# Optimization experiments

Measured on AMD Instinct MI355X. Metric: run time of the kernel, lower is better.

Reference implementation:

```python
import math
import jax, jax.numpy as jnp
import numpy as np

L, B, D = 2048, 8, 1024
Z, H, N = 128, 2048, 16


def setup_inputs() -> dict:
    key = jax.random.key(0)
    ks = jax.random.split(key, 16)
    s = 0.02
    inp = {
        "x": jax.random.normal(ks[0], (L, B, D), jnp.float32),
        "ln_w": jnp.ones((D,), jnp.float32),
        "ln_b": jnp.zeros((D,), jnp.float32),
        "v_w": jax.random.normal(ks[1], (H, D), jnp.float32) * s,
        "v_b": jnp.zeros((H,), jnp.float32),
        "mx_w": jax.random.normal(ks[2], (Z + H + 2 * D, D), jnp.float32) * s,
        "mx_b": jnp.zeros((Z + H + 2 * D,), jnp.float32),
        "h_w": jax.random.normal(ks[3], (D, H), jnp.float32) * s,
        "h_b": jnp.zeros((D,), jnp.float32),
        "qk_gamma": jnp.ones((2, Z), jnp.float32) + jax.random.normal(ks[4], (2, Z), jnp.float32) * s,
        "qk_beta": jax.random.normal(ks[5], (2, Z), jnp.float32) * s,
        "ema_delta": jax.random.normal(ks[6], (D, N, 1), jnp.float32),
        "ema_alpha": jax.random.normal(ks[7], (D, N, 1), jnp.float32),
        "ema_beta": jax.random.normal(ks[8], (D, N, 1), jnp.float32) * s,
        "ema_gamma": jax.random.normal(ks[9], (D, N), jnp.float32) * s,
        "ema_omega": jax.random.normal(ks[10], (D,), jnp.float32) * s,
        "rb_alpha": jax.random.normal(ks[11], (1, Z), jnp.float32) * s,
        "rb_beta": jax.random.normal(ks[12], (1, Z), jnp.float32) * s,
    }
    return inp


def _rotary_bias(rb_alpha, rb_beta, seq_len, z):
    # RotaryRelativePositionalBias.forward(seq_len) -> (L, L)
    half = z // 2
    freqs = jnp.exp(jnp.arange(half, dtype=jnp.float32) * (-math.log(10000.0) / half))
    pos = jnp.arange(seq_len, dtype=jnp.float32)[:, None] * freqs[None, :]  # (L, half)
    sin, cos = jnp.sin(pos), jnp.cos(pos)

    def rot(w):  # (1, Z) -> (L, Z)
        we = jnp.broadcast_to(w, (seq_len, z))
        w1, w2 = we[:, :half], we[:, half:]
        return jnp.concatenate([w1 * cos - w2 * sin, w2 * cos + w1 * sin], axis=1)

    return rot(rb_alpha) @ rot(rb_beta).T  # (L, L)


def _ema(xn, ema_delta, ema_alpha, ema_beta, ema_gamma, ema_omega):
    # xn: (L, B, D) -> damped multi-head EMA via FFT causal conv (MEGA MultiHeadEMA)
    seq_len = xn.shape[0]
    p = jax.nn.sigmoid(ema_delta)           # (D, N, 1)
    a = jax.nn.sigmoid(ema_alpha)           # (D, N, 1)
    q = 1.0 - p * a                         # (D, N, 1)
    t = jnp.arange(seq_len, dtype=jnp.float32)[None, None, :]
    kern = (p * ema_beta) * jnp.exp(t * jnp.log(q))          # (D, N, L)
    scale = math.sqrt(1.0 / kern.shape[1])
    k_dl = jnp.einsum("dnl,dn->dl", kern, ema_gamma * scale)  # (D, L)
    xt = jnp.transpose(xn, (1, 2, 0))        # (B, D, L)
    nfft = 2 * seq_len
    kf = jnp.fft.rfft(k_dl, n=nfft)          # (D, F)
    xf = jnp.fft.rfft(xt, n=nfft)            # (B, D, F)
    conv = jnp.fft.irfft(xf * kf, n=nfft)[..., :seq_len]      # (B, D, L)
    return jax.nn.silu(jnp.transpose(conv, (2, 0, 1)) + xn * ema_omega)  # (L, B, D)


def reference(x, ln_w, ln_b, v_w, v_b, mx_w, mx_b, h_w, h_b, qk_gamma, qk_beta,
              ema_delta, ema_alpha, ema_beta, ema_gamma, ema_omega, rb_alpha, rb_beta):
    seq_len, bsz, d = x.shape
    residual = x
    # prenorm LayerNorm
    mu = jnp.mean(x, axis=-1, keepdims=True)
    var = jnp.mean(jnp.square(x - mu), axis=-1, keepdims=True)
    xn = (x - mu) * jax.lax.rsqrt(var + 1e-5) * ln_w + ln_b

    v = jax.nn.silu(xn @ v_w.T + v_b)                          # (L, B, H)
    mx = _ema(xn, ema_delta, ema_alpha, ema_beta, ema_gamma, ema_omega)
    base = mx @ mx_w.T + mx_b                                  # (L, B, Z+H+2D)
    u = jax.nn.sigmoid(base[..., :d])                          # update gate
    zr = jax.nn.silu(base[..., d:d + Z + H])
    hx = base[..., d + Z + H:]
    z, r = zr[..., :Z], zr[..., Z:]                            # (L,B,Z), (L,B,H)
    z2 = z[:, :, None, :] * qk_gamma + qk_beta                 # (L, B, 2, Z)
    q = jnp.transpose(z2[:, :, 0], (1, 0, 2)) * (Z ** -0.5)    # (B, L, Z)
    k = jnp.transpose(z2[:, :, 1], (1, 0, 2))                  # (B, L, Z)
    vb = jnp.transpose(v, (1, 0, 2))                           # (B, L, H)

    bias = _rotary_bias(rb_alpha, rb_beta, seq_len, Z)         # (L, L)
    attn = jax.nn.softmax(jnp.einsum("blz,bmz->blm", q, k) + bias, axis=-1)
    h = jnp.transpose(jnp.einsum("blm,bmh->blh", attn, vb), (1, 0, 2))  # (L, B, H)
    h = jax.nn.silu(hx + (h * r) @ h_w.T + h_b)                # (L, B, D)
    return residual + u * (h - residual)
```

## Files before the change

### kernel.cpp

```cpp
#include <hip/hip_runtime.h>
#include <cstdint>
#include <cstddef>

typedef __bf16 bf16;
typedef __bf16 bf16x8 __attribute__((ext_vector_type(8)));
typedef float  f32x4  __attribute__((ext_vector_type(4)));

#define DEVI static __device__ __forceinline__

DEVI float fsigmoid(float x) { return 1.0f / (1.0f + __expf(-x)); }
DEVI float fsilu(float x)    { return x / (1.0f + __expf(-x)); }

DEVI unsigned short b16bits(float v) { bf16 h = (bf16)v; return __builtin_bit_cast(unsigned short, h); }
DEVI float lo16f(unsigned int w) { return __builtin_bit_cast(float, w << 16); }
DEVI float hi16f(unsigned int w) { return __builtin_bit_cast(float, w & 0xffff0000u); }

DEVI float waveRedSum(float v) {
#pragma unroll
  for (int o = 32; o > 0; o >>= 1) v += __shfl_xor(v, o, 64);
  return v;
}
DEVI float waveRedMax(float v) {
#pragma unroll
  for (int o = 32; o > 0; o >>= 1) v = fmaxf(v, __shfl_xor(v, o, 64));
  return v;
}

DEVI void xcd_swizzle(int& bx, int& by) {
  const int gx = gridDim.x, gy = gridDim.y;
  const int nwg = gx * gy;
  const int flat = blockIdx.y * gx + blockIdx.x;
  const int xcd = flat & 7;
  const int rem = nwg & 7;
  const int q = nwg >> 3;
  const int base = (xcd < rem) ? xcd * (q + 1) : rem * (q + 1) + (xcd - rem) * q;
  const int swz = base + (flat >> 3);
  bx = swz % gx;
  by = swz / gx;
}

struct alignas(8) B4 { bf16 x, y, z, w; };

__global__ __launch_bounds__(256) void k_copyout(const float* __restrict__ x, float* __restrict__ o)
{
  const long i = (long)blockIdx.x * 256 + threadIdx.x;
  ((float4*)o)[i] = ((const float4*)x)[i];
}

__global__ __launch_bounds__(256) void k_lnstats(const float* __restrict__ x, float* __restrict__ stats)
{
  const long t = blockIdx.x;
  const int tid = threadIdx.x;
  const float4 v = ((const float4*)(x + t * 1024))[tid];
  float s  = v.x + v.y + v.z + v.w;
  float s2 = v.x * v.x + v.y * v.y + v.z * v.z + v.w * v.w;
  __shared__ float red[2][4];
  s = waveRedSum(s);
  s2 = waveRedSum(s2);
  const int wv = tid >> 6, ln = tid & 63;
  if (ln == 0) { red[0][wv] = s; red[1][wv] = s2; }
  __syncthreads();
  if (tid == 0) {
    s  = red[0][0] + red[0][1] + red[0][2] + red[0][3];
    s2 = red[1][0] + red[1][1] + red[1][2] + red[1][3];
    const float mu  = s * (1.0f / 1024.0f);
    const float var = s2 * (1.0f / 1024.0f) - mu * mu;
    stats[2 * t]     = mu;
    stats[2 * t + 1] = rsqrtf(var + 1e-5f);
  }
}

__global__ __launch_bounds__(256) void k_cvt(const float* __restrict__ in, bf16* __restrict__ out, int n4)
{
  const int i = blockIdx.x * 256 + threadIdx.x;
  if (i >= n4) return;
  const float4 v = ((const float4*)in)[i];
  B4 h; h.x = (bf16)v.x; h.y = (bf16)v.y; h.z = (bf16)v.z; h.w = (bf16)v.w;
  ((B4*)out)[i] = h;
}

__global__ __launch_bounds__(256) void k_ema_coeff(
    const float* __restrict__ de, const float* __restrict__ al,
    const float* __restrict__ be, const float* __restrict__ ga,
    float* __restrict__ qv, float* __restrict__ cv)
{
  const int i = blockIdx.x * 256 + threadIdx.x;
  const int d = i >> 4, n = i & 15;
  const float p = 1.0f / (1.0f + expf(-de[i]));
  const float a = 1.0f / (1.0f + expf(-al[i]));
  qv[n * 1024 + d] = 1.0f - p * a;
  cv[n * 1024 + d] = p * be[i] * ga[i] * 0.25f;
}

__global__ __launch_bounds__(256) void k_ema_scan1(
    const float* __restrict__ x, const float* __restrict__ stats,
    const float* __restrict__ lnw, const float* __restrict__ lnb,
    const float* __restrict__ qv, float* __restrict__ scan)
{
  const int d = blockIdx.x * 256 + threadIdx.x;
  const int b = blockIdx.y, c = blockIdx.z;
  float q[16], s[16];
#pragma unroll
  for (int n = 0; n < 16; ++n) { q[n] = qv[n * 1024 + d]; s[n] = 0.0f; }
  const float wd = lnw[d], bd = lnb[d];
  const float* xp = x + (long)b * 1024 + d;
  const int l0 = c * 128;
  for (int j0 = 0; j0 < 128; j0 += 8) {
    float xr[8]; float2 st[8];
#pragma unroll
    for (int i = 0; i < 8; ++i) {
      const int l = l0 + j0 + i;
      xr[i] = xp[(long)l * 8192];
      st[i] = ((const float2*)stats)[(long)l * 8 + b];
    }
#pragma unroll
    for (int i = 0; i < 8; ++i) {
      const float xv = (xr[i] - st[i].x) * st[i].y * wd + bd;
#pragma unroll
      for (int n = 0; n < 16; ++n) s[n] = fmaf(q[n], s[n], xv);
    }
  }
  float* sp = scan + ((((long)c * 8 + b) * 1024) + d) * 16;
#pragma unroll
  for (int n = 0; n < 16; ++n) sp[n] = s[n];
}

__global__ __launch_bounds__(256) void k_ema_scan2(
    const float* __restrict__ qv, float* __restrict__ scan)
{
  const int i = blockIdx.x * 256 + threadIdx.x;
  const int n = i & 15, d = (i >> 4) & 1023, b = i >> 14;
  const float q = qv[n * 1024 + d];
  const float q2 = q * q, q4 = q2 * q2, q8 = q4 * q4;
  const float q16 = q8 * q8, q32 = q16 * q16, q64 = q32 * q32, q128 = q64 * q64;
  float carry = 0.0f;
#pragma unroll
  for (int c = 0; c < 16; ++c) {
    const long off = ((((long)c * 8 + b) * 1024) + d) * 16 + n;
    const float t = scan[off];
    scan[off] = carry;
    carry = fmaf(q128, carry, t);
  }
}

__global__ __launch_bounds__(256) void k_ema_apply(
    const float* __restrict__ x, const float* __restrict__ stats,
    const float* __restrict__ lnw, const float* __restrict__ lnb,
    const float* __restrict__ qv, const float* __restrict__ cv,
    const float* __restrict__ omega, const float* __restrict__ scan,
    bf16* __restrict__ mx)
{
  const int d = blockIdx.x * 256 + threadIdx.x;
  const int b = blockIdx.y, c = blockIdx.z;
  float q[16], cc[16], s[16];
  const float* sp = scan + ((((long)c * 8 + b) * 1024) + d) * 16;
#pragma unroll
  for (int n = 0; n < 16; ++n) {
    q[n] = qv[n * 1024 + d];
    cc[n] = cv[n * 1024 + d];
    s[n] = sp[n];
  }
  const float om = omega[d], wd = lnw[d], bd = lnb[d];
  const float* xp = x + (long)b * 1024 + d;
  bf16* mp = mx + (long)b * 1024 + d;
  const int l0 = c * 128;
  for (int j0 = 0; j0 < 128; j0 += 8) {
    float xr[8]; float2 st[8];
#pragma unroll
    for (int i = 0; i < 8; ++i) {
      const int l = l0 + j0 + i;
      xr[i] = xp[(long)l * 8192];
      st[i] = ((const float2*)stats)[(long)l * 8 + b];
    }
#pragma unroll
    for (int i = 0; i < 8; ++i) {
      const float xv = (xr[i] - st[i].x) * st[i].y * wd + bd;
      float p0 = 0.f, p1 = 0.f, p2 = 0.f, p3 = 0.f;
#pragma unroll
      for (int n = 0; n < 16; n += 4) {
        s[n]     = fmaf(q[n],     s[n],     xv);
        s[n + 1] = fmaf(q[n + 1], s[n + 1], xv);
        s[n + 2] = fmaf(q[n + 2], s[n + 2], xv);
        s[n + 3] = fmaf(q[n + 3], s[n + 3], xv);
        p0 = fmaf(cc[n],     s[n],     p0);
        p1 = fmaf(cc[n + 1], s[n + 1], p1);
        p2 = fmaf(cc[n + 2], s[n + 2], p2);
        p3 = fmaf(cc[n + 3], s[n + 3], p3);
      }
      const float pre = fmaf(xv, om, (p0 + p1) + (p2 + p3));
      mp[(long)(l0 + j0 + i) * 8192] = (bf16)fsilu(pre);
    }
  }
}

__global__ __launch_bounds__(64) void k_rotfill(
    const float* __restrict__ rba, const float* __restrict__ rbb,
    bf16* __restrict__ Qp, bf16* __restrict__ Kp)
{
  const int l = blockIdx.x, zi = threadIdx.x;
  const float fr = __expf(-0.14391156831212787f * (float)zi);
  const float pos = (float)l * fr;
  const float sn = sinf(pos), cs = cosf(pos);
  const float a1 = rba[zi], a2 = rba[64 + zi];
  const float b1 = rbb[zi], b2 = rbb[64 + zi];
  const bf16 qa = (bf16)(a1 * cs - a2 * sn);
  const bf16 qb = (bf16)(a2 * cs + a1 * sn);
  const bf16 ka = (bf16)(b1 * cs - b2 * sn);
  const bf16 kb = (bf16)(b2 * cs + b1 * sn);
#pragma unroll
  for (int b = 0; b < 8; ++b) {
    const long base = ((long)b * 2048 + l) * 256;
    Qp[base + 128 + zi] = qa;
    Qp[base + 192 + zi] = qb;
    Kp[base + 128 + zi] = ka;
    Kp[base + 192 + zi] = kb;
  }
}

__global__ __launch_bounds__(256) void k_softmax(float* __restrict__ S)
{
  const long row = blockIdx.x;
  float* sp = S + row * 2048;
  const int tid = threadIdx.x;
  float vals[8];
  float mx = -1e30f;
#pragma unroll
  for (int i = 0; i < 8; ++i) { vals[i] = sp[i * 256 + tid]; mx = fmaxf(mx, vals[i]); }
  __shared__ float red[4];
  mx = waveRedMax(mx);
  const int wv = tid >> 6, ln = tid & 63;
  if (ln == 0) red[wv] = mx;
  __syncthreads();
  mx = fmaxf(fmaxf(red[0], red[1]), fmaxf(red[2], red[3]));
  float sum = 0.f;
#pragma unroll
  for (int i = 0; i < 8; ++i) { vals[i] = __expf(vals[i] - mx); sum += vals[i]; }
  __syncthreads();
  sum = waveRedSum(sum);
  if (ln == 0) red[wv] = sum;
  __syncthreads();
  sum = red[0] + red[1] + red[2] + red[3];
  const float inv = 1.0f / sum;
  bf16* pp = (bf16*)sp;
#pragma unroll
  for (int i = 0; i < 8; ++i) pp[i * 256 + tid] = (bf16)(vals[i] * inv);
}

__global__ __launch_bounds__(1024) void k_vtrans8(
    const bf16* __restrict__ v, bf16* __restrict__ vt, const int loff)
{
  __shared__ bf16 tile[32][33];
  const int l0 = blockIdx.x * 32, h0 = blockIdx.y * 32, b = blockIdx.z;
  const int tx = threadIdx.x, ty = threadIdx.y;
  tile[ty][tx] = v[((long)(l0 + ty) * 8 + b) * 2048 + h0 + tx];
  __syncthreads();
  vt[((long)b * 2048 + h0 + ty) * 2048 + loff + l0 + tx] = tile[tx][ty];
}

DEVI void gload16(const void* g, void* l) {
  __builtin_amdgcn_global_load_lds(
      (__attribute__((address_space(1))) void*)(void*)g,
      (__attribute__((address_space(3))) void*)l, 16, 0, 0);
}

template<int EPI>
__global__ __launch_bounds__(256) void k_gemm_bt(
    const bf16* __restrict__ A, const bf16* __restrict__ Bm,
    const int K, const int lda, const int ldb, const int coladd,
    const float* __restrict__ bias,
    void* __restrict__ o0, void* __restrict__ o1, void* __restrict__ o2, void* __restrict__ o3,
    const void* __restrict__ e0, const void* __restrict__ e1, const void* __restrict__ e2)
{
  __shared__ alignas(16) bf16 As[128 * 64];
  __shared__ alignas(16) bf16 Bs[128 * 64];
  const int tid = threadIdx.x;
  const int wave = tid >> 6, lane = tid & 63;
  const int wm = wave >> 1, wn = wave & 1;
  int bx, by;
  xcd_swizzle(bx, by);
  const int tm = by * 128, tn = bx * 128;
  const int fr = lane & 15, kg = lane >> 4;

  f32x4 acc[4][4];
  const f32x4 z4 = {0.0f, 0.0f, 0.0f, 0.0f};
#pragma unroll
  for (int i = 0; i < 4; ++i)
#pragma unroll
    for (int j = 0; j < 4; ++j) acc[i][j] = z4;

  const int srow = wave * 8 + (lane >> 3);
  const int scol = ((lane & 7) ^ (lane >> 3)) * 8;
  const long arow = (long)(tm + srow);
  const long brow = (long)(tn + srow);
  const int swR = (fr & 7) << 3;

  for (int k0 = 0; k0 < K; k0 += 64) {
    __syncthreads();
#pragma unroll
    for (int cc = 0; cc < 4; ++cc) {
      gload16(A + (arow + cc * 32) * lda + k0 + scol, As + cc * 2048 + wave * 512);
      gload16(Bm + (brow + cc * 32) * ldb + k0 + scol, Bs + cc * 2048 + wave * 512);
    }
    __syncthreads();
    bf16x8 af[2][4], bfv[2][4];
#pragma unroll
    for (int ks = 0; ks < 2; ++ks)
#pragma unroll
      for (int i = 0; i < 4; ++i) {
        af[ks][i]  = *(const bf16x8*)&As[(wm * 64 + i * 16 + fr) * 64 + ((ks * 32 + kg * 8) ^ swR)];
        bfv[ks][i] = *(const bf16x8*)&Bs[(wn * 64 + i * 16 + fr) * 64 + ((ks * 32 + kg * 8) ^ swR)];
      }
#pragma unroll
    for (int ks = 0; ks < 2; ++ks)
#pragma unroll
      for (int i = 0; i < 4; ++i)
#pragma unroll
        for (int j = 0; j < 4; ++j)
          acc[i][j] = __builtin_amdgcn_mfma_f32_16x16x32_bf16(af[ks][i], bfv[ks][j], acc[i][j], 0, 0, 0);
  }

#pragma unroll
  for (int i = 0; i < 4; ++i) {
#pragma unroll
    for (int j = 0; j < 4; ++j) {
#pragma unroll
      for (int rr = 0; rr < 4; ++rr) {
        const int row = tm + wm * 64 + i * 16 + kg * 4 + rr;
        const int col = coladd + tn + wn * 64 + j * 16 + fr;
        const float a = acc[i][j][rr];
        if constexpr (EPI == 1) {
          const float tv = a + bias[col];
          if (col < 1024) {
            ((unsigned short*)o0)[((long)row * 1024 + col) * 2] = b16bits(fsigmoid(tv));
          } else if (col < 1152) {
            const int zi = col - 1024;
            const float zval = fsilu(tv);
            const float qq = (zval * ((const float*)e0)[zi] + ((const float*)e1)[zi]) * 0.08838834764831845f;
            const float kk =  zval * ((const float*)e0)[128 + zi] + ((const float*)e1)[128 + zi];
            const long base = ((long)(row & 7) * 2048 + (row >> 3)) * 256 + zi;
            ((bf16*)o2)[base] = (bf16)qq;
            ((bf16*)o3)[base] = (bf16)kk;
          } else if (col < 3200) {
            ((bf16*)o1)[(long)row * 2048 + (col - 1152)] = (bf16)fsilu(tv);
          } else {
            ((unsigned short*)o0)[((long)row * 1024 + (col - 3200)) * 2 + 1] = b16bits(tv);
          }
        } else if constexpr (EPI == 2) {
          ((float*)o0)[(long)row * 2048 + col] = a;
        } else if constexpr (EPI == 3) {
          const long idx = (long)row * 16384 + col;
          const float rv = (float)((const bf16*)e0)[idx];
          ((bf16*)o0)[idx] = (bf16)(a * rv);
        } else if constexpr (EPI == 4) {
          const long idx = (long)row * 1024 + col;
          const unsigned int w = ((const unsigned int*)o0)[idx];
          const float uv = lo16f(w), hxv = hi16f(w);
          const float hval = fsilu(hxv + a + bias[col]);
          const float xv = ((const float*)e1)[idx];
          ((float*)o0)[idx] = xv + uv * (hval - xv);
        }
      }
    }
  }
}

__global__ __launch_bounds__(256) void k_gemm_lnA(
    const float* __restrict__ x, const float* __restrict__ stats,
    const float* __restrict__ lnw, const float* __restrict__ lnb,
    const bf16* __restrict__ Bm, const float* __restrict__ bias,
    bf16* __restrict__ out)
{
  __shared__ alignas(16) bf16 As[128 * 64];
  __shared__ alignas(16) bf16 Bs[128 * 64];
  __shared__ float smu[128], srs[128];
  const int tid = threadIdx.x;
  const int wave = tid >> 6, lane = tid & 63;
  const int wm = wave >> 1, wn = wave & 1;
  int bx, by;
  xcd_swizzle(bx, by);
  const int tm = by * 128, tn = bx * 128;
  const int fr = lane & 15, kg = lane >> 4;
  if (tid < 128) {
    smu[tid] = stats[2 * (long)(tm + tid)];
    srs[tid] = stats[2 * (long)(tm + tid) + 1];
  }

  f32x4 acc[4][4];
  const f32x4 z4 = {0.0f, 0.0f, 0.0f, 0.0f};
#pragma unroll
  for (int i = 0; i < 4; ++i)
#pragma unroll
    for (int j = 0; j < 4; ++j) acc[i][j] = z4;

  const int srow = wave * 8 + (lane >> 3);
  const int scol = ((lane & 7) ^ (lane >> 3)) * 8;
  const long brow = (long)(tn + srow);
  const int swR = (fr & 7) << 3;
  const int ar = tid & 127, ah = (tid >> 7) * 32;
  const float* xrow = x + (long)(tm + ar) * 1024 + ah;

  for (int k0 = 0; k0 < 1024; k0 += 64) {
    __syncthreads();
#pragma unroll
    for (int cc = 0; cc < 4; ++cc)
      gload16(Bm + (brow + cc * 32) * 1024 + k0 + scol, Bs + cc * 2048 + wave * 512);
    {
      const float mu = smu[ar], rs = srs[ar];
      bf16 tmp[32];
#pragma unroll
      for (int i = 0; i < 8; ++i) {
        const float4 xv = ((const float4*)(xrow + k0))[i];
        const float4 wv = ((const float4*)(lnw + k0 + ah))[i];
        const float4 bv = ((const float4*)(lnb + k0 + ah))[i];
        tmp[i * 4 + 0] = (bf16)((xv.x - mu) * rs * wv.x + bv.x);
        tmp[i * 4 + 1] = (bf16)((xv.y - mu) * rs * wv.y + bv.y);
        tmp[i * 4 + 2] = (bf16)((xv.z - mu) * rs * wv.z + bv.z);
        tmp[i * 4 + 3] = (bf16)((xv.w - mu) * rs * wv.w + bv.w);
      }
      const int sw = (ar & 7) << 3;
#pragma unroll
      for (int i = 0; i < 4; ++i)
        *(bf16x8*)&As[ar * 64 + ((ah + i * 8) ^ sw)] = *(const bf16x8*)&tmp[i * 8];
    }
    __syncthreads();
    bf16x8 af[2][4], bfv[2][4];
#pragma unroll
    for (int ks = 0; ks < 2; ++ks)
#pragma unroll
      for (int i = 0; i < 4; ++i) {
        const int ar2 = wm * 64 + i * 16 + fr;
        af[ks][i]  = *(const bf16x8*)&As[ar2 * 64 + ((ks * 32 + kg * 8) ^ ((ar2 & 7) << 3))];
        bfv[ks][i] = *(const bf16x8*)&Bs[(wn * 64 + i * 16 + fr) * 64 + ((ks * 32 + kg * 8) ^ swR)];
      }
#pragma unroll
    for (int ks = 0; ks < 2; ++ks)
#pragma unroll
      for (int i = 0; i < 4; ++i)
#pragma unroll
        for (int j = 0; j < 4; ++j)
          acc[i][j] = __builtin_amdgcn_mfma_f32_16x16x32_bf16(af[ks][i], bfv[ks][j], acc[i][j], 0, 0, 0);
  }

#pragma unroll
  for (int i = 0; i < 4; ++i)
#pragma unroll
    for (int j = 0; j < 4; ++j)
#pragma unroll
      for (int rr = 0; rr < 4; ++rr) {
        const int row = tm + wm * 64 + i * 16 + kg * 4 + rr;
        const int col = tn + wn * 64 + j * 16 + fr;
        out[(long)row * 2048 + col] = (bf16)fsilu(acc[i][j][rr] + bias[col]);
      }
}

extern "C" void kernel_launch(void* const* d_in, const int* in_sizes, int n_in,
                              void* d_out, int out_size, void* d_ws, size_t ws_size,
                              hipStream_t stream)
{
  const float* x    = (const float*)d_in[0];
  const float* ln_w = (const float*)d_in[1];
  const float* ln_b = (const float*)d_in[2];
  const float* v_w  = (const float*)d_in[3];
  const float* v_b  = (const float*)d_in[4];
  const float* mx_w = (const float*)d_in[5];
  const float* mx_b = (const float*)d_in[6];
  const float* h_w  = (const float*)d_in[7];
  const float* h_b  = (const float*)d_in[8];
  const float* qk_g = (const float*)d_in[9];
  const float* qk_b = (const float*)d_in[10];
  const float* e_de = (const float*)d_in[11];
  const float* e_al = (const float*)d_in[12];
  const float* e_be = (const float*)d_in[13];
  const float* e_ga = (const float*)d_in[14];
  const float* e_om = (const float*)d_in[15];
  const float* rb_a = (const float*)d_in[16];
  const float* rb_b = (const float*)d_in[17];

  const size_t MiB = 1048576UL;
  if (ws_size < 160 * MiB) {
    k_copyout<<<16384, 256, 0, stream>>>(x, (float*)d_out);
    return;
  }

  char* ws = (char*)d_ws;
  bf16*  rbuf  = (bf16*)(ws + 0 * MiB);
  bf16*  v_t   = (bf16*)(ws + 64 * MiB);
  bf16*  mxw_h = (bf16*)(ws + 64 * MiB);
  bf16*  mxb   = (bf16*)(ws + 73 * MiB);
  float* qv    = (float*)(ws + 105 * MiB);
  float* cv    = (float*)(ws + 105 * MiB + 65536);
  bf16*  Qp    = (bf16*)(ws + 128 * MiB);
  bf16*  hw_h  = (bf16*)(ws + 128 * MiB);
  bf16*  Kp    = (bf16*)(ws + 136 * MiB);
  float* Sbuf  = (float*)(ws + 144 * MiB);
  bf16*  vw_h  = (bf16*)(ws + 144 * MiB);
  float* scanb = (float*)(ws + 148 * MiB);
  bf16*  vbufe = (bf16*)(ws + 148 * MiB);
  float* stats = (float*)(ws + 156 * MiB);

  k_lnstats<<<16384, 256, 0, stream>>>(x, stats);
  k_cvt<<<2048, 256, 0, stream>>>(v_w, vw_h, 524288);
  k_cvt<<<4224, 256, 0, stream>>>(mx_w, mxw_h, 1081344);
  k_ema_coeff<<<64, 256, 0, stream>>>(e_de, e_al, e_be, e_ga, qv, cv);

  k_ema_scan1<<<dim3(4, 8, 16), 256, 0, stream>>>(x, stats, ln_w, ln_b, qv, scanb);
  k_ema_scan2<<<512, 256, 0, stream>>>(qv, scanb);
  k_ema_apply<<<dim3(4, 8, 16), 256, 0, stream>>>(x, stats, ln_w, ln_b, qv, cv, e_om, scanb, mxb);

  k_gemm_bt<1><<<dim3(33, 128, 1), 256, 0, stream>>>(mxb, mxw_h, 1024, 1024, 1024, 0,
      mx_b, d_out, (void*)rbuf, (void*)Qp, (void*)Kp, (const void*)qk_g, (const void*)qk_b, nullptr);
  k_rotfill<<<2048, 64, 0, stream>>>(rb_a, rb_b, Qp, Kp);

  for (int e = 0; e < 8; ++e) {
    k_gemm_lnA<<<dim3(16, 16, 1), 256, 0, stream>>>(x + (long)e * 2048 * 1024, stats + (long)e * 4096,
        ln_w, ln_b, vw_h, v_b, vbufe);
    k_vtrans8<<<dim3(8, 64, 8), dim3(32, 32), 0, stream>>>(vbufe, v_t, e * 256);
  }

  for (int b = 0; b < 8; ++b) {
    const bf16* Ab = Qp + (long)b * 524288;
    const bf16* Bb = Kp + (long)b * 524288;
    k_gemm_bt<2><<<dim3(16, 16, 1), 256, 0, stream>>>(Ab, Bb, 256, 256, 256, 0,
        nullptr, (void*)Sbuf, nullptr, nullptr, nullptr, nullptr, nullptr, nullptr);
    k_softmax<<<2048, 256, 0, stream>>>(Sbuf);
    bf16* hrp = rbuf + (long)b * 2048;
    k_gemm_bt<3><<<dim3(16, 16, 1), 256, 0, stream>>>((const bf16*)Sbuf, v_t + (long)b * 4194304,
        2048, 4096, 2048, 0, nullptr, (void*)hrp, nullptr, nullptr, nullptr, (const void*)hrp, nullptr, nullptr);
  }

  k_cvt<<<2048, 256, 0, stream>>>(h_w, hw_h, 524288);

  k_gemm_bt<4><<<dim3(8, 128, 1), 256, 0, stream>>>(rbuf, hw_h, 2048, 2048, 2048, 0,
      h_b, d_out, nullptr, nullptr, nullptr, nullptr, (const void*)x, nullptr);
}
```

Measured before the change: 1.468 ms.

## Use 256x256 double-buffered GEMM kernel for mx and output projections

Adds a new GEMM kernel with 256x256 tiles, 512 threads and double-buffered LDS that prefetches the next K slice while computing the current one. It is used for the large mx projection (padded to 4352 columns, with a memset zeroing the pad rows) and for the final h projection. The old 128x128 kernel is kept for the attention GEMMs. The larger tiles raise data reuse and hide global load latency, at the cost of 128KB of LDS per block, higher register pressure and a partial last column tile that wastes some work.

New measurement: 1.540 ms. 4.9% more time.

```diff
diff --git a/kernel.cpp b/kernel.cpp
--- a/kernel.cpp
+++ b/kernel.cpp
@@ -263,72 +263,95 @@
       (__attribute__((address_space(3))) void*)l, 16, 0, 0);
 }
 
+DEVI void drain_vmem() {
+  asm volatile("s_waitcnt vmcnt(0)" ::: "memory");
+}
+
 template<int EPI>
-__global__ __launch_bounds__(256) void k_gemm_bt(
+__global__ __launch_bounds__(512, 2) void k_gemm256(
     const bf16* __restrict__ A, const bf16* __restrict__ Bm,
-    const int K, const int lda, const int ldb, const int coladd,
+    const int K, const int lda, const int ldb, const int ncols,
     const float* __restrict__ bias,
     void* __restrict__ o0, void* __restrict__ o1, void* __restrict__ o2, void* __restrict__ o3,
-    const void* __restrict__ e0, const void* __restrict__ e1, const void* __restrict__ e2)
-{
-  __shared__ alignas(16) bf16 As[128 * 64];
-  __shared__ alignas(16) bf16 Bs[128 * 64];
+    const void* __restrict__ e0, const void* __restrict__ e1)
+{
+  __shared__ alignas(16) bf16 As[2][16384];
+  __shared__ alignas(16) bf16 Bs[2][16384];
   const int tid = threadIdx.x;
-  const int wave = tid >> 6, lane = tid & 63;
-  const int wm = wave >> 1, wn = wave & 1;
+  const int wid = tid >> 6, lane = tid & 63;
+  const int wm = wid >> 2, wn = wid & 3;
   int bx, by;
   xcd_swizzle(bx, by);
-  const int tm = by * 128, tn = bx * 128;
+  const int tm = by * 256, tn = bx * 256;
   const int fr = lane & 15, kg = lane >> 4;
-
-  f32x4 acc[4][4];
+  const int swR = (fr & 7) << 3;
+
+  f32x4 acc[8][4];
   const f32x4 z4 = {0.0f, 0.0f, 0.0f, 0.0f};
 #pragma unroll
-  for (int i = 0; i < 4; ++i)
+  for (int i = 0; i < 8; ++i)
 #pragma unroll
     for (int j = 0; j < 4; ++j) acc[i][j] = z4;
 
-  const int srow = wave * 8 + (lane >> 3);
-  const int scol = ((lane & 7) ^ (lane >> 3)) * 8;
-  const long arow = (long)(tm + srow);
-  const long brow = (long)(tn + srow);
-  const int swR = (fr & 7) << 3;
-
-  for (int k0 = 0; k0 < K; k0 += 64) {
+  int srow[4], scolv[4];
+#pragma unroll
+  for (int g = 0; g < 4; ++g) {
+    const int cidx = g * 512 + tid;
+    srow[g] = cidx >> 3;
+    scolv[g] = ((cidx & 7) ^ (srow[g] & 7)) * 8;
+  }
+
+  const int nt = K >> 6;
+#pragma unroll
+  for (int g = 0; g < 4; ++g) {
+    gload16(A + (long)(tm + srow[g]) * lda + scolv[g], &As[0][g * 4096 + wid * 512]);
+    gload16(Bm + (long)(tn + srow[g]) * ldb + scolv[g], &Bs[0][g * 4096 + wid * 512]);
+  }
+  drain_vmem();
+  __syncthreads();
+
+  for (int t = 0; t < nt; ++t) {
+    const int cur = t & 1;
+    if (t + 1 < nt) {
+      const int k1 = (t + 1) << 6;
+#pragma unroll
+      for (int g = 0; g < 4; ++g) {
+        gload16(A + (long)(tm + srow[g]) * lda + k1 + scolv[g], &As[cur ^ 1][g * 4096 + wid * 512]);
+        gload16(Bm + (long)(tn + srow[g]) * ldb + k1 + scolv[g], &Bs[cur ^ 1][g * 4096 + wid * 512]);
+      }
+    }
+    const bf16* Ab = &As[cur][0];
+    const bf16* Bb = &Bs[cur][0];
+#pragma unroll
+    for (int ks = 0; ks < 2; ++ks) {
+      bf16x8 af[8], bfv[4];
+#pragma unroll
+      for (int j = 0; j < 4; ++j)
+        bfv[j] = *(const bf16x8*)&Bb[(wn * 64 + j * 16 + fr) * 64 + ((ks * 32 + kg * 8) ^ swR)];
+#pragma unroll
+      for (int i = 0; i < 8; ++i)
+        af[i] = *(const bf16x8*)&Ab[(wm * 128 + i * 16 + fr) * 64 + ((ks * 32 + kg * 8) ^ swR)];
+#pragma unroll
+      for (int i = 0; i < 8; ++i)
+#pragma unroll
+        for (int j = 0; j < 4; ++j)
+          acc[i][j] = __builtin_amdgcn_mfma_f32_16x16x32_bf16(af[i], bfv[j], acc[i][j], 0, 0, 0);
+    }
+    drain_vmem();
     __syncthreads();
-#pragma unroll
-    for (int cc = 0; cc < 4; ++cc) {
-      gload16(A + (arow + cc * 32) * lda + k0 + scol, As + cc * 2048 + wave * 512);
-      gload16(Bm + (brow + cc * 32) * ldb + k0 + scol, Bs + cc * 2048 + wave * 512);
-    }
-    __syncthreads();
-    bf16x8 af[2][4], bfv[2][4];
-#pragma unroll
-    for (int ks = 0; ks < 2; ++ks)
-#pragma unroll
-      for (int i = 0; i < 4; ++i) {
-        af[ks][i]  = *(const bf16x8*)&As[(wm * 64 + i * 16 + fr) * 64 + ((ks * 32 + kg * 8) ^ swR)];
-        bfv[ks][i] = *(const bf16x8*)&Bs[(wn * 64 + i * 16 + fr) * 64 + ((ks * 32 + kg * 8) ^ swR)];
-      }
-#pragma unroll
-    for (int ks = 0; ks < 2; ++ks)
-#pragma unroll
-      for (int i = 0; i < 4; ++i)
-#pragma unroll
-        for (int j = 0; j < 4; ++j)
-          acc[i][j] = __builtin_amdgcn_mfma_f32_16x16x32_bf16(af[ks][i], bfv[ks][j], acc[i][j], 0, 0, 0);
-  }
-
-#pragma unroll
-  for (int i = 0; i < 4; ++i) {
+  }
+
+#pragma unroll
+  for (int i = 0; i < 8; ++i) {
 #pragma unroll
     for (int j = 0; j < 4; ++j) {
 #pragma unroll
       for (int rr = 0; rr < 4; ++rr) {
-        const int row = tm + wm * 64 + i * 16 + kg * 4 + rr;
-        const int col = coladd + tn + wn * 64 + j * 16 + fr;
+        const int row = tm + wm * 128 + i * 16 + kg * 4 + rr;
+        const int col = tn + wn * 64 + j * 16 + fr;
         const float a = acc[i][j][rr];
         if constexpr (EPI == 1) {
+          if (col >= ncols) continue;
           const float tv = a + bias[col];
           if (col < 1024) {
             ((unsigned short*)o0)[((long)row * 1024 + col) * 2] = b16bits(fsigmoid(tv));
@@ -345,12 +368,6 @@
           } else {
             ((unsigned short*)o0)[((long)row * 1024 + (col - 3200)) * 2 + 1] = b16bits(tv);
           }
-        } else if constexpr (EPI == 2) {
-          ((float*)o0)[(long)row * 2048 + col] = a;
-        } else if constexpr (EPI == 3) {
-          const long idx = (long)row * 16384 + col;
-          const float rv = (float)((const bf16*)e0)[idx];
-          ((bf16*)o0)[idx] = (bf16)(a * rv);
         } else if constexpr (EPI == 4) {
           const long idx = (long)row * 1024 + col;
           const unsigned int w = ((const unsigned int*)o0)[idx];
@@ -358,6 +375,83 @@
           const float hval = fsilu(hxv + a + bias[col]);
           const float xv = ((const float*)e1)[idx];
           ((float*)o0)[idx] = xv + uv * (hval - xv);
+        }
+      }
+    }
+  }
+}
+
+template<int EPI>
+__global__ __launch_bounds__(256) void k_gemm_bt(
+    const bf16* __restrict__ A, const bf16* __restrict__ Bm,
+    const int K, const int lda, const int ldb, const int coladd,
+    const float* __restrict__ bias,
+    void* __restrict__ o0, void* __restrict__ o1, void* __restrict__ o2, void* __restrict__ o3,
+    const void* __restrict__ e0, const void* __restrict__ e1, const void* __restrict__ e2)
+{
+  __shared__ alignas(16) bf16 As[128 * 64];
+  __shared__ alignas(16) bf16 Bs[128 * 64];
+  const int tid = threadIdx.x;
+  const int wave = tid >> 6, lane = tid & 63;
+  const int wm = wave >> 1, wn = wave & 1;
+  int bx, by;
+  xcd_swizzle(bx, by);
+  const int tm = by * 128, tn = bx * 128;
+  const int fr = lane & 15, kg = lane >> 4;
+
+  f32x4 acc[4][4];
+  const f32x4 z4 = {0.0f, 0.0f, 0.0f, 0.0f};
+#pragma unroll
+  for (int i = 0; i < 4; ++i)
+#pragma unroll
+    for (int j = 0; j < 4; ++j) acc[i][j] = z4;
+
+  const int srow = wave * 8 + (lane >> 3);
+  const int scol = ((lane & 7) ^ (lane >> 3)) * 8;
+  const long arow = (long)(tm + srow);
+  const long brow = (long)(tn + srow);
+  const int swR = (fr & 7) << 3;
+
+  for (int k0 = 0; k0 < K; k0 += 64) {
+    __syncthreads();
+#pragma unroll
+    for (int cc = 0; cc < 4; ++cc) {
+      gload16(A + (arow + cc * 32) * lda + k0 + scol, As + cc * 2048 + wave * 512);
+      gload16(Bm + (brow + cc * 32) * ldb + k0 + scol, Bs + cc * 2048 + wave * 512);
+    }
+    __syncthreads();
+    bf16x8 af[2][4], bfv[2][4];
+#pragma unroll
+    for (int ks = 0; ks < 2; ++ks)
+#pragma unroll
+      for (int i = 0; i < 4; ++i) {
+        af[ks][i]  = *(const bf16x8*)&As[(wm * 64 + i * 16 + fr) * 64 + ((ks * 32 + kg * 8) ^ swR)];
+        bfv[ks][i] = *(const bf16x8*)&Bs[(wn * 64 + i * 16 + fr) * 64 + ((ks * 32 + kg * 8) ^ swR)];
+      }
+#pragma unroll
+    for (int ks = 0; ks < 2; ++ks)
+#pragma unroll
+      for (int i = 0; i < 4; ++i)
+#pragma unroll
+        for (int j = 0; j < 4; ++j)
+          acc[i][j] = __builtin_amdgcn_mfma_f32_16x16x32_bf16(af[ks][i], bfv[ks][j], acc[i][j], 0, 0, 0);
+  }
+
+#pragma unroll
+  for (int i = 0; i < 4; ++i) {
+#pragma unroll
+    for (int j = 0; j < 4; ++j) {
+#pragma unroll
+      for (int rr = 0; rr < 4; ++rr) {
+        const int row = tm + wm * 64 + i * 16 + kg * 4 + rr;
+        const int col = coladd + tn + wn * 64 + j * 16 + fr;
+        const float a = acc[i][j][rr];
+        if constexpr (EPI == 2) {
+          ((float*)o0)[(long)row * 2048 + col] = a;
+        } else if constexpr (EPI == 3) {
+          const long idx = (long)row * 16384 + col;
+          const float rv = (float)((const bf16*)e0)[idx];
+          ((bf16*)o0)[idx] = (bf16)(a * rv);
         }
       }
     }
@@ -500,6 +594,7 @@
 
   k_lnstats<<<16384, 256, 0, stream>>>(x, stats);
   k_cvt<<<2048, 256, 0, stream>>>(v_w, vw_h, 524288);
+  hipMemsetAsync(mxw_h + 4224L * 1024, 0, 128L * 1024 * 2, stream);
   k_cvt<<<4224, 256, 0, stream>>>(mx_w, mxw_h, 1081344);
   k_ema_coeff<<<64, 256, 0, stream>>>(e_de, e_al, e_be, e_ga, qv, cv);
 
@@ -507,8 +602,8 @@
   k_ema_scan2<<<512, 256, 0, stream>>>(qv, scanb);
   k_ema_apply<<<dim3(4, 8, 16), 256, 0, stream>>>(x, stats, ln_w, ln_b, qv, cv, e_om, scanb, mxb);
 
-  k_gemm_bt<1><<<dim3(33, 128, 1), 256, 0, stream>>>(mxb, mxw_h, 1024, 1024, 1024, 0,
-      mx_b, d_out, (void*)rbuf, (void*)Qp, (void*)Kp, (const void*)qk_g, (const void*)qk_b, nullptr);
+  k_gemm256<1><<<dim3(17, 64, 1), 512, 0, stream>>>(mxb, mxw_h, 1024, 1024, 1024, 4224,
+      mx_b, d_out, (void*)rbuf, (void*)Qp, (void*)Kp, (const void*)qk_g, (const void*)qk_b);
   k_rotfill<<<2048, 64, 0, stream>>>(rb_a, rb_b, Qp, Kp);
 
   for (int e = 0; e < 8; ++e) {
@@ -530,6 +625,6 @@
 
   k_cvt<<<2048, 256, 0, stream>>>(h_w, hw_h, 524288);
 
-  k_gemm_bt<4><<<dim3(8, 128, 1), 256, 0, stream>>>(rbuf, hw_h, 2048, 2048, 2048, 0,
-      h_b, d_out, nullptr, nullptr, nullptr, nullptr, (const void*)x, nullptr);
-}
+  k_gemm256<4><<<dim3(4, 64, 1), 512, 0, stream>>>(rbuf, hw_h, 2048, 2048, 2048, 1024,
+      h_b, d_out, nullptr, nullptr, nullptr, nullptr, (const void*)x);
+}
```
